# Optimization experiments

Measured on AMD Instinct MI355X. Metric: run time of the kernel, lower is better.

The kernel has to match this reference:

```python
import math
import jax, jax.numpy as jnp
import numpy as np

TEMPERATURE = 1.0  # matches init kwarg

S, B, T, D = 16, 4, 1024, 2048


def setup_inputs() -> dict:
    key = jax.random.key(0)
    k1, k2 = jax.random.split(key)
    layer_query = jax.random.normal(k1, (D,), dtype=jnp.float32)
    source_bank = jax.random.normal(k2, (S, B, T, D), dtype=jnp.float32)
    return {"layer_query": layer_query, "source_bank": source_bank, "num_sources": S}


def reference(layer_query, source_bank, num_sources):
    # RMSNorm over last dim of the key bank (torch F.rms_norm with eps=None
    # uses the dtype's machine epsilon)
    eps = jnp.finfo(source_bank.dtype).eps
    ms = jnp.mean(jnp.square(source_bank), axis=-1, keepdims=True)  # [s,b,t,1]
    keys = source_bank * jax.lax.rsqrt(ms + eps)
    d = source_bank.shape[-1]
    scale = 1.0 / (math.sqrt(d) * TEMPERATURE)
    query = layer_query.astype(source_bank.dtype)
    scores = jnp.einsum('d,sbtd->sbt', query, keys) * scale  # [s,b,t]
    weights = jax.nn.softmax(scores, axis=0)                 # softmax over sources
    mixed = jnp.einsum('sbt,sbtd->btd', weights, source_bank)
    return mixed
```

## Files before the change

### kernel.cpp

```cpp
#include <hip/hip_runtime.h>


#define NSRC 16
#define NB   4
#define NT   1024
#define ND   2048

__global__ __launch_bounds__(512, 4)
void dar_reg_kernel(const float* __restrict__ q,
                    const float* __restrict__ bank,
                    float* __restrict__ out) {
    __shared__ float2 red[8][NSRC];

    const int tid  = threadIdx.x;
    const int wave = tid >> 6;
    const int lane = tid & 63;
    const int bt   = blockIdx.x;

    const float4* bt_base = reinterpret_cast<const float4*>(bank)
                          + (size_t)bt * (ND / 4) + tid;
    const float4 qv = reinterpret_cast<const float4*>(q)[tid];

    float4 xs[NSRC];
    #pragma unroll
    for (int s = 0; s < NSRC; ++s)
        xs[s] = bt_base[(size_t)s * (NB * NT) * (ND / 4)];

    #pragma unroll
    for (int s = 0; s < NSRC; ++s) {
        const float4 v = xs[s];
        float p2 = v.x * v.x + v.y * v.y + v.z * v.z + v.w * v.w;
        float pq = qv.x * v.x + qv.y * v.y + qv.z * v.z + qv.w * v.w;
        #pragma unroll
        for (int m = 32; m >= 1; m >>= 1) {
            p2 += __shfl_xor(p2, m, 64);
            pq += __shfl_xor(pq, m, 64);
        }
        if (lane == 0) red[wave][s] = make_float2(p2, pq);
    }
    __syncthreads();

    const int sl = lane & 15;
    float p2 = 0.0f, pq = 0.0f;
    #pragma unroll
    for (int w = 0; w < 8; ++w) {
        const float2 r = red[w][sl];
        p2 += r.x;
        pq += r.y;
    }
    const float score = pq * rsqrtf(p2 * (1.0f / ND) + 1.1920928955078125e-07f)
                      * 0.022097086912079608f;

    float mx = score;
    #pragma unroll
    for (int m = 1; m <= 8; m <<= 1) mx = fmaxf(mx, __shfl_xor(mx, m, 64));
    const float es = __expf(score - mx);
    float sum = es;
    #pragma unroll
    for (int m = 1; m <= 8; m <<= 1) sum += __shfl_xor(sum, m, 64);
    const float inv = 1.0f / sum;

    float4 acc = make_float4(0.0f, 0.0f, 0.0f, 0.0f);
    #pragma unroll
    for (int s = 0; s < NSRC; ++s) {
        const float ws = __shfl(es, s, 64) * inv;
        acc.x += ws * xs[s].x;
        acc.y += ws * xs[s].y;
        acc.z += ws * xs[s].z;
        acc.w += ws * xs[s].w;
    }
    reinterpret_cast<float4*>(out + (size_t)bt * ND)[tid] = acc;
}

extern "C" void kernel_launch(void* const* d_in, const int* in_sizes, int n_in,
                              void* d_out, int out_size, void* d_ws, size_t ws_size,
                              hipStream_t stream) {
    const float* q    = (const float*)d_in[0];
    const float* bank = (const float*)d_in[1];
    float* out        = (float*)d_out;

    dim3 grid(NB * NT);
    dim3 block(512);
    dar_reg_kernel<<<grid, block, 0, stream>>>(q, bank, out);
}
```

Baseline: 115.0 us.

## Hold bank values as fp16 in registers and raise occupancy with nontemporal access

Each source's float4 is packed into two fp16 pairs held in registers, so the weighted mix reads from half as many registers. This lets launch bounds move from 4 to 6 blocks per CU for more memory parallelism. Loads and the output store become nontemporal, and loads are issued in groups of four with the norm and dot products computed right after each group. The fp16 rounding (round-toward-zero) of the mixed values costs accuracy and may break tolerance.

```diff
diff --git a/kernel.cpp b/kernel.cpp
--- a/kernel.cpp
+++ b/kernel.cpp
@@ -1,4 +1,5 @@
 #include <hip/hip_runtime.h>
+#include <stdint.h>
 
 
 #define NSRC 16
@@ -6,10 +7,13 @@
 #define NT   1024
 #define ND   2048
 
-__global__ __launch_bounds__(512, 4)
-void dar_reg_kernel(const float* __restrict__ q,
-                    const float* __restrict__ bank,
-                    float* __restrict__ out) {
+typedef float  f32x4 __attribute__((ext_vector_type(4)));
+typedef __fp16 h16x2 __attribute__((ext_vector_type(2)));
+
+__global__ __launch_bounds__(512, 6)
+void dar_reg16_kernel(const float* __restrict__ q,
+                      const float* __restrict__ bank,
+                      float* __restrict__ out) {
     __shared__ float2 red[8][NSRC];
 
     const int tid  = threadIdx.x;
@@ -17,38 +21,57 @@
     const int lane = tid & 63;
     const int bt   = blockIdx.x;
 
-    const float4* bt_base = reinterpret_cast<const float4*>(bank)
-                          + (size_t)bt * (ND / 4) + tid;
-    const float4 qv = reinterpret_cast<const float4*>(q)[tid];
+    const f32x4* bt_base = reinterpret_cast<const f32x4*>(bank)
+                         + (size_t)bt * (ND / 4) + tid;
+    const f32x4 qv = reinterpret_cast<const f32x4*>(q)[tid];
 
-    float4 xs[NSRC];
+    const size_t SSTRIDE = (size_t)(NB * NT) * (ND / 4);
+
+    uint2 xh[NSRC];
+    float p2[NSRC], pq[NSRC];
+
     #pragma unroll
-    for (int s = 0; s < NSRC; ++s)
-        xs[s] = bt_base[(size_t)s * (NB * NT) * (ND / 4)];
+    for (int g = 0; g < 4; ++g) {
+        f32x4 v[4];
+        #pragma unroll
+        for (int k = 0; k < 4; ++k)
+            v[k] = __builtin_nontemporal_load(bt_base + (size_t)(g * 4 + k) * SSTRIDE);
+        #pragma unroll
+        for (int k = 0; k < 4; ++k) {
+            const int s = g * 4 + k;
+            p2[s] = v[k].x * v[k].x + v[k].y * v[k].y + v[k].z * v[k].z + v[k].w * v[k].w;
+            pq[s] = qv.x * v[k].x + qv.y * v[k].y + qv.z * v[k].z + qv.w * v[k].w;
+            const h16x2 lo = __builtin_amdgcn_cvt_pkrtz(v[k].x, v[k].y);
+            const h16x2 hi = __builtin_amdgcn_cvt_pkrtz(v[k].z, v[k].w);
+            xh[s].x = __builtin_bit_cast(uint32_t, lo);
+            xh[s].y = __builtin_bit_cast(uint32_t, hi);
+        }
+    }
 
     #pragma unroll
     for (int s = 0; s < NSRC; ++s) {
-        const float4 v = xs[s];
-        float p2 = v.x * v.x + v.y * v.y + v.z * v.z + v.w * v.w;
-        float pq = qv.x * v.x + qv.y * v.y + qv.z * v.z + qv.w * v.w;
         #pragma unroll
         for (int m = 32; m >= 1; m >>= 1) {
-            p2 += __shfl_xor(p2, m, 64);
-            pq += __shfl_xor(pq, m, 64);
+            p2[s] += __shfl_xor(p2[s], m, 64);
+            pq[s] += __shfl_xor(pq[s], m, 64);
         }
-        if (lane == 0) red[wave][s] = make_float2(p2, pq);
+    }
+    if (lane == 0) {
+        #pragma unroll
+        for (int s = 0; s < NSRC; ++s)
+            red[wave][s] = make_float2(p2[s], pq[s]);
     }
     __syncthreads();
 
     const int sl = lane & 15;
-    float p2 = 0.0f, pq = 0.0f;
+    float tp2 = 0.0f, tpq = 0.0f;
     #pragma unroll
     for (int w = 0; w < 8; ++w) {
         const float2 r = red[w][sl];
-        p2 += r.x;
-        pq += r.y;
+        tp2 += r.x;
+        tpq += r.y;
     }
-    const float score = pq * rsqrtf(p2 * (1.0f / ND) + 1.1920928955078125e-07f)
+    const float score = tpq * rsqrtf(tp2 * (1.0f / ND) + 1.1920928955078125e-07f)
                       * 0.022097086912079608f;
 
     float mx = score;
@@ -58,18 +81,22 @@
     float sum = es;
     #pragma unroll
     for (int m = 1; m <= 8; m <<= 1) sum += __shfl_xor(sum, m, 64);
-    const float inv = 1.0f / sum;
+    const float esn = es / sum;
 
-    float4 acc = make_float4(0.0f, 0.0f, 0.0f, 0.0f);
+    float ax = 0.0f, ay = 0.0f, az = 0.0f, aw = 0.0f;
     #pragma unroll
     for (int s = 0; s < NSRC; ++s) {
-        const float ws = __shfl(es, s, 64) * inv;
-        acc.x += ws * xs[s].x;
-        acc.y += ws * xs[s].y;
-        acc.z += ws * xs[s].z;
-        acc.w += ws * xs[s].w;
+        const float ws = __shfl(esn, s, 64);
+        const h16x2 lo = __builtin_bit_cast(h16x2, xh[s].x);
+        const h16x2 hi = __builtin_bit_cast(h16x2, xh[s].y);
+        ax += ws * (float)lo.x;
+        ay += ws * (float)lo.y;
+        az += ws * (float)hi.x;
+        aw += ws * (float)hi.y;
     }
-    reinterpret_cast<float4*>(out + (size_t)bt * ND)[tid] = acc;
+    f32x4 r;
+    r.x = ax; r.y = ay; r.z = az; r.w = aw;
+    __builtin_nontemporal_store(r, reinterpret_cast<f32x4*>(out) + (size_t)bt * (ND / 4) + tid);
 }
 
 extern "C" void kernel_launch(void* const* d_in, const int* in_sizes, int n_in,
@@ -81,5 +108,5 @@
 
     dim3 grid(NB * NT);
     dim3 block(512);
-    dar_reg_kernel<<<grid, block, 0, stream>>>(q, bank, out);
+    dar_reg16_kernel<<<grid, block, 0, stream>>>(q, bank, out);
 }
```

After: 256.6 us. +123.0%, slower.
